# Kernel optimization log

Hardware: AMD Instinct MI355X
Metric: run time of the kernel (lower is better)

Reference implementation:

```python
import jax, jax.numpy as jnp
import numpy as np


def setup_inputs() -> dict:
    key = jax.random.key(0)
    B, N = 8192, 2048
    f = jax.random.normal(key, (B, N), dtype=jnp.float32)
    return {"f": f, "num_stocks": N}


def reference(f, num_stocks):
    N = num_stocks
    half = N // 2
    # l = sum of top half scores minus sum of bottom half scores, per row
    l = jnp.sum(f[:, half:], axis=1) - jnp.sum(f[:, :half], axis=1)
    col = jnp.arange(N)
    neg_inf = jnp.asarray(-jnp.inf, f.dtype)

    def step(acc, i):
        # window f[:, i:N-i] expressed as a mask (jit-friendly, fixed shapes)
        mask = (col >= i) & (col < N - i)
        fm = jnp.where(mask, f, neg_inf)
        fn = jnp.where(mask, -f, neg_inf)
        acc = acc + jax.nn.logsumexp(fm, axis=1) + jax.nn.logsumexp(fn, axis=1)
        return acc, None

    l, _ = jax.lax.scan(step, l, jnp.arange(half))
    return jnp.mean(l)
```

## Files before the change

kernel.cpp:

```cpp
#include <hip/hip_runtime.h>


#define NCOLS 2048
#define HALF  1024
#define TPB   256

__global__ __launch_bounds__(TPB) void closs_row_kernel(const float* __restrict__ f,
                                                        float* __restrict__ partial) {
    const int row = blockIdx.x;
    const float* fr = f + (size_t)row * NCOLS;
    const int t    = threadIdx.x;
    const int lane = t & 63;
    const int wave = t >> 6;

    const int jbase = HALF - 4 - 4 * t;
    const float4 lo = *reinterpret_cast<const float4*>(fr + jbase);
    const float4 hi = *reinterpret_cast<const float4*>(fr + (NCOLS - 4 - jbase));
    const float* lop = reinterpret_cast<const float*>(&lo);
    const float* hip_ = reinterpret_cast<const float*>(&hi);

    float pp[4], pm[4];
    float sp = 0.f, sm = 0.f;
    float lsum = 0.f;
    #pragma unroll
    for (int q = 0; q < 4; ++q) {
        const float a = lop[3 - q];
        const float b = hip_[q];
        const float ep = __expf(a) + __expf(b);
        const float em = __expf(-a) + __expf(-b);
        sp += ep; pp[q] = sp;
        sm += em; pm[q] = sm;
        lsum += b - a;
    }

    float ip = sp, im = sm;
    #pragma unroll
    for (int d = 1; d < 64; d <<= 1) {
        const float op = __shfl_up(ip, d, 64);
        const float om = __shfl_up(im, d, 64);
        if (lane >= d) { ip += op; im += om; }
    }

    __shared__ float wtp[4], wtm[4], cw[4];
    if (lane == 63) { wtp[wave] = ip; wtm[wave] = im; }
    __syncthreads();
    float offp = ip - sp;
    float offm = im - sm;
    #pragma unroll
    for (int w = 0; w < 3; ++w) {
        if (w < wave) { offp += wtp[w]; offm += wtm[w]; }
    }

    float c = lsum;
    #pragma unroll
    for (int q = 0; q < 4; ++q) {
        c += __logf(offp + pp[q]) + __logf(offm + pm[q]);
    }

    #pragma unroll
    for (int d = 32; d > 0; d >>= 1) c += __shfl_down(c, d, 64);
    if (lane == 0) cw[wave] = c;
    __syncthreads();
    if (t == 0) partial[row] = cw[0] + cw[1] + cw[2] + cw[3];
}

__global__ __launch_bounds__(256) void closs_reduce_kernel(const float* __restrict__ partial,
                                                           float* __restrict__ out,
                                                           int n, double inv) {
    __shared__ double sd[256];
    double s = 0.0;
    for (int i = threadIdx.x; i < n; i += 256) s += (double)partial[i];
    sd[threadIdx.x] = s;
    __syncthreads();
    for (int step = 128; step > 0; step >>= 1) {
        if (threadIdx.x < step) sd[threadIdx.x] += sd[threadIdx.x + step];
        __syncthreads();
    }
    if (threadIdx.x == 0) out[0] = (float)(sd[0] * inv);
}

extern "C" void kernel_launch(void* const* d_in, const int* in_sizes, int n_in,
                              void* d_out, int out_size, void* d_ws, size_t ws_size,
                              hipStream_t stream) {
    const float* f = (const float*)d_in[0];
    const int Brows = in_sizes[0] / NCOLS;
    float* partial = (float*)d_ws;

    closs_row_kernel<<<Brows, TPB, 0, stream>>>(f, partial);
    closs_reduce_kernel<<<1, 256, 0, stream>>>(partial, (float*)d_out,
                                               Brows, 1.0 / (double)Brows);
}
```

Measured before the change: 102.0 us.

## Map one wavefront per row and cut transcendentals in prefix log-sum-exp

Each row is now handled by a single 64-lane wavefront processing 16 symmetric pairs per lane, so the cross-wave shared-memory scan and both block barriers go away. exp(-a)+exp(-b) is computed as (ea+eb)/(ea*eb) with a hardware reciprocal, and the two logs are merged into one log of a product, halving both exp and log counts. The risks are overflow or underflow in ea*eb and in the product for extreme inputs, higher register pressure, and the assumption that the row count is divisible by four. The final reduce kernel also switches to float4 loads.

```diff
diff --git a/kernel.cpp b/kernel.cpp
--- a/kernel.cpp
+++ b/kernel.cpp
@@ -3,33 +3,40 @@
 
 #define NCOLS 2048
 #define HALF  1024
-#define TPB   256
+#define PAIRS 16
 
-__global__ __launch_bounds__(TPB) void closs_row_kernel(const float* __restrict__ f,
+__global__ __launch_bounds__(256) void closs_row_kernel(const float* __restrict__ f,
                                                         float* __restrict__ partial) {
-    const int row = blockIdx.x;
+    const int lane = threadIdx.x & 63;
+    const int row  = blockIdx.x * 4 + (threadIdx.x >> 6);
     const float* fr = f + (size_t)row * NCOLS;
-    const int t    = threadIdx.x;
-    const int lane = t & 63;
-    const int wave = t >> 6;
 
-    const int jbase = HALF - 4 - 4 * t;
-    const float4 lo = *reinterpret_cast<const float4*>(fr + jbase);
-    const float4 hi = *reinterpret_cast<const float4*>(fr + (NCOLS - 4 - jbase));
-    const float* lop = reinterpret_cast<const float*>(&lo);
-    const float* hip_ = reinterpret_cast<const float*>(&hi);
+    const float* lo_base = fr + (HALF - PAIRS - PAIRS * lane);
+    const float* hi_base = fr + (HALF + PAIRS * lane);
 
-    float pp[4], pm[4];
-    float sp = 0.f, sm = 0.f;
-    float lsum = 0.f;
+    float lov[PAIRS], hiv[PAIRS];
     #pragma unroll
-    for (int q = 0; q < 4; ++q) {
-        const float a = lop[3 - q];
-        const float b = hip_[q];
-        const float ep = __expf(a) + __expf(b);
-        const float em = __expf(-a) + __expf(-b);
-        sp += ep; pp[q] = sp;
-        sm += em; pm[q] = sm;
+    for (int q = 0; q < PAIRS / 4; ++q) {
+        const float4 lv = *reinterpret_cast<const float4*>(lo_base + 4 * q);
+        const float4 hv = *reinterpret_cast<const float4*>(hi_base + 4 * q);
+        lov[4 * q + 0] = lv.x; lov[4 * q + 1] = lv.y;
+        lov[4 * q + 2] = lv.z; lov[4 * q + 3] = lv.w;
+        hiv[4 * q + 0] = hv.x; hiv[4 * q + 1] = hv.y;
+        hiv[4 * q + 2] = hv.z; hiv[4 * q + 3] = hv.w;
+    }
+
+    float pp[PAIRS], pm[PAIRS];
+    float sp = 0.f, sm = 0.f, lsum = 0.f;
+    #pragma unroll
+    for (int p = 0; p < PAIRS; ++p) {
+        const float a  = lov[PAIRS - 1 - p];
+        const float b  = hiv[p];
+        const float ea = __expf(a);
+        const float eb = __expf(b);
+        const float ep = ea + eb;
+        const float em = ep * __builtin_amdgcn_rcpf(ea * eb);
+        sp += ep; pp[p] = sp;
+        sm += em; pm[p] = sm;
         lsum += b - a;
     }
 
@@ -40,43 +47,37 @@
         const float om = __shfl_up(im, d, 64);
         if (lane >= d) { ip += op; im += om; }
     }
-
-    __shared__ float wtp[4], wtm[4], cw[4];
-    if (lane == 63) { wtp[wave] = ip; wtm[wave] = im; }
-    __syncthreads();
-    float offp = ip - sp;
-    float offm = im - sm;
-    #pragma unroll
-    for (int w = 0; w < 3; ++w) {
-        if (w < wave) { offp += wtp[w]; offm += wtm[w]; }
-    }
+    const float offp = ip - sp;
+    const float offm = im - sm;
 
     float c = lsum;
     #pragma unroll
-    for (int q = 0; q < 4; ++q) {
-        c += __logf(offp + pp[q]) + __logf(offm + pm[q]);
+    for (int p = 0; p < PAIRS; ++p) {
+        c += __logf((offp + pp[p]) * (offm + pm[p]));
     }
 
     #pragma unroll
-    for (int d = 32; d > 0; d >>= 1) c += __shfl_down(c, d, 64);
-    if (lane == 0) cw[wave] = c;
-    __syncthreads();
-    if (t == 0) partial[row] = cw[0] + cw[1] + cw[2] + cw[3];
+    for (int d = 32; d > 0; d >>= 1) c += __shfl_xor(c, d, 64);
+    if (lane == 0) partial[row] = c;
 }
 
 __global__ __launch_bounds__(256) void closs_reduce_kernel(const float* __restrict__ partial,
                                                            float* __restrict__ out,
                                                            int n, double inv) {
     __shared__ double sd[256];
+    const int t = threadIdx.x;
     double s = 0.0;
-    for (int i = threadIdx.x; i < n; i += 256) s += (double)partial[i];
-    sd[threadIdx.x] = s;
+    for (int i = t * 4; i < n; i += 256 * 4) {
+        const float4 v = *reinterpret_cast<const float4*>(partial + i);
+        s += (double)v.x + (double)v.y + (double)v.z + (double)v.w;
+    }
+    sd[t] = s;
     __syncthreads();
     for (int step = 128; step > 0; step >>= 1) {
-        if (threadIdx.x < step) sd[threadIdx.x] += sd[threadIdx.x + step];
+        if (t < step) sd[t] += sd[t + step];
         __syncthreads();
     }
-    if (threadIdx.x == 0) out[0] = (float)(sd[0] * inv);
+    if (t == 0) out[0] = (float)(sd[0] * inv);
 }
 
 extern "C" void kernel_launch(void* const* d_in, const int* in_sizes, int n_in,
@@ -86,7 +87,7 @@
     const int Brows = in_sizes[0] / NCOLS;
     float* partial = (float*)d_ws;
 
-    closs_row_kernel<<<Brows, TPB, 0, stream>>>(f, partial);
+    closs_row_kernel<<<Brows / 4, 256, 0, stream>>>(f, partial);
     closs_reduce_kernel<<<1, 256, 0, stream>>>(partial, (float*)d_out,
                                                Brows, 1.0 / (double)Brows);
 }
```

Result: faster. 95.78 us (-6.1%).
